# Kernel tuning notes

Measured on AMD Instinct MI355X. Metric: run time of the kernel, lower is better.

## Reference

```python
import jax, jax.numpy as jnp
import numpy as np

B, S, E, H = 1, 4096, 768, 12
D = E // H  # head_dim = 64


def setup_inputs() -> dict:
    key = jax.random.key(0)
    ks = jax.random.split(key, 9)
    s = 1.0 / np.sqrt(E)
    return {
        "x": jax.random.normal(ks[0], (B, S, E), dtype=jnp.float32),
        "Wq": jax.random.uniform(ks[1], (E, E), jnp.float32, -s, s),
        "bq": jax.random.uniform(ks[2], (E,), jnp.float32, -s, s),
        "Wk": jax.random.uniform(ks[3], (E, E), jnp.float32, -s, s),
        "bk": jax.random.uniform(ks[4], (E,), jnp.float32, -s, s),
        "Wv": jax.random.uniform(ks[5], (E, E), jnp.float32, -s, s),
        "bv": jax.random.uniform(ks[6], (E,), jnp.float32, -s, s),
        "Wo": jax.random.uniform(ks[7], (E, E), jnp.float32, -s, s),
        "bo": jax.random.uniform(ks[8], (E,), jnp.float32, -s, s),
    }


def reference(x, Wq, bq, Wk, bk, Wv, bv, Wo, bo):
    b, s, e = x.shape
    # QKV projections, split heads -> [b, h, s, d]
    def split(t):
        return t.reshape(b, s, H, D).transpose(0, 2, 1, 3)
    q = split(x @ Wq.T + bq)
    k = split(x @ Wk.T + bk)
    v = split(x @ Wv.T + bv)
    scores = jnp.einsum("bhqd,bhkd->bhqk", q, k) / jnp.sqrt(jnp.float32(D))
    attn = jax.nn.softmax(scores, axis=-1)  # dropout is identity in eval
    out = jnp.einsum("bhqk,bhkd->bhqd", attn, v)
    out = out.transpose(0, 2, 1, 3).reshape(b, s, e)
    return out @ Wo.T + bo
```

## Files before the change

kernel.cpp:

```cpp
#include <hip/hip_runtime.h>
#include <hip/hip_bf16.h>
#include <math.h>

#define SEQ 4096
#define EDIM 768
#define NHEAD 12
#define HDIM 64
#define SE (SEQ * EDIM)
#define WMAT (EDIM * EDIM)
#define QSCALE 0.180336880111f

typedef __attribute__((ext_vector_type(8))) __bf16 bf16x8;
typedef __attribute__((ext_vector_type(4))) float f32x4;
typedef __attribute__((ext_vector_type(8))) unsigned short u16x8;
typedef __attribute__((ext_vector_type(4))) unsigned short u16x4;
typedef unsigned short ushort_t;
typedef unsigned int uint_t;

#define MFMA16(a, b, c) __builtin_amdgcn_mfma_f32_16x16x32_bf16(a, b, c, 0, 0, 0)
#define GLOAD_LDS16(g, l)                                          \
  __builtin_amdgcn_global_load_lds(                                \
      (const __attribute__((address_space(1))) void*)(g),          \
      (__attribute__((address_space(3))) void*)(l), 16, 0, 0)

__device__ __forceinline__ unsigned short bfbits(float x) {
  return __builtin_bit_cast(unsigned short, (__bf16)x);
}
__device__ __forceinline__ void split1(float x, unsigned short* h,
                                       unsigned short* l) {
  __bf16 hb = (__bf16)x;
  *h = __builtin_bit_cast(unsigned short, hb);
  *l = __builtin_bit_cast(unsigned short, (__bf16)(x - (float)hb));
}
__device__ __forceinline__ bf16x8 ones8() {
  u16x8 u;
#pragma unroll
  for (int e = 0; e < 8; ++e) u[e] = 0x3F80;
  return __builtin_bit_cast(bf16x8, u);
}
__device__ __forceinline__ float exp2_hw(float x) {
  float r;
  asm("v_exp_f32 %0, %1" : "=v"(r) : "v"(x));
  return r;
}

__global__ __launch_bounds__(256) void wprep_kernel(
    const float* __restrict__ W0, const float* __restrict__ W1,
    const float* __restrict__ W2, const float* __restrict__ W3,
    ushort_t* __restrict__ WB, ushort_t* __restrict__ WOH,
    ushort_t* __restrict__ WOL) {
  const int m = blockIdx.y;
  const float* src = (m == 0) ? W0 : (m == 1) ? W1 : (m == 2) ? W2 : W3;
  const size_t i = ((size_t)blockIdx.x * 256 + threadIdx.x) * 8;
  float4 a = *(const float4*)(src + i);
  float4 b = *(const float4*)(src + i + 4);
  float fv[8] = {a.x, a.y, a.z, a.w, b.x, b.y, b.z, b.w};
  if (m < 3) {
    u16x8 hh;
#pragma unroll
    for (int e = 0; e < 8; ++e) hh[e] = bfbits(fv[e]);
    *(u16x8*)(WB + (size_t)m * WMAT + i) = hh;
  } else {
    u16x8 hh, ll;
#pragma unroll
    for (int e = 0; e < 8; ++e) {
      unsigned short x, y;
      split1(fv[e], &x, &y);
      hh[e] = x;
      ll[e] = y;
    }
    *(u16x8*)(WOH + i) = hh;
    *(u16x8*)(WOL + i) = ll;
  }
}

__global__ __launch_bounds__(256) void xprep_kernel(
    const float* __restrict__ x, ushort_t* __restrict__ xb) {
  const size_t i = ((size_t)blockIdx.x * 256 + threadIdx.x) * 8;
  float4 a = *(const float4*)(x + i);
  float4 b = *(const float4*)(x + i + 4);
  float fv[8] = {a.x, a.y, a.z, a.w, b.x, b.y, b.z, b.w};
  u16x8 hh;
#pragma unroll
  for (int e = 0; e < 8; ++e) hh[e] = bfbits(fv[e]);
  *(u16x8*)(xb + i) = hh;
}

__global__ __launch_bounds__(256) void qkv_kernel(
    const ushort_t* __restrict__ XB, const ushort_t* __restrict__ WB,
    const float* __restrict__ bq, const float* __restrict__ bk,
    const float* __restrict__ bv, ushort_t* __restrict__ QB,
    ushort_t* __restrict__ KB, ushort_t* __restrict__ VT) {
  __shared__ __align__(16) ushort_t AS[128][32];
  __shared__ __align__(16) ushort_t BS[128][32];

  const int z = blockIdx.z;
  const ushort_t* Bmat = WB + (size_t)z * WMAT;
  const float* bias = (z == 0) ? bq : (z == 1) ? bk : bv;
  ushort_t* outp = (z == 0) ? QB : (z == 1) ? KB : VT;
  const float scale = (z == 0) ? QSCALE : 1.0f;

  const int t = threadIdx.x;
  const int lane = t & 63;
  const int w = t >> 6;
  const int tn = t & 15;
  const int g = (t >> 4) & 3;
  const int wr = w >> 1, wc = w & 1;
  const int m0 = blockIdx.x * 128;
  const int n0 = blockIdx.y * 128;

  f32x4 acc[4][4];
#pragma unroll
  for (int mi = 0; mi < 4; ++mi)
#pragma unroll
    for (int nj = 0; nj < 4; ++nj) acc[mi][nj] = (f32x4){0.f, 0.f, 0.f, 0.f};

  const int crow = lane >> 2;
  const int ccol = (lane & 3) * 8;

  for (int k0 = 0; k0 < EDIM; k0 += 32) {
    __syncthreads();
#pragma unroll
    for (int i = 0; i < 2; ++i) {
      const int ch = w + 4 * i;
      const int row = ch * 16 + crow;
      GLOAD_LDS16(XB + (size_t)(m0 + row) * EDIM + k0 + ccol, &AS[ch * 16][0]);
      GLOAD_LDS16(Bmat + (size_t)(n0 + row) * EDIM + k0 + ccol, &BS[ch * 16][0]);
    }
    __syncthreads();

    bf16x8 ah[4], bh[4];
#pragma unroll
    for (int mi = 0; mi < 4; ++mi)
      ah[mi] = __builtin_bit_cast(
          bf16x8, *(const u16x8*)&AS[wr * 64 + mi * 16 + tn][8 * g]);
#pragma unroll
    for (int nj = 0; nj < 4; ++nj)
      bh[nj] = __builtin_bit_cast(
          bf16x8, *(const u16x8*)&BS[wc * 64 + nj * 16 + tn][8 * g]);
#pragma unroll
    for (int mi = 0; mi < 4; ++mi)
#pragma unroll
      for (int nj = 0; nj < 4; ++nj)
        acc[mi][nj] = MFMA16(ah[mi], bh[nj], acc[mi][nj]);
  }

#pragma unroll
  for (int mi = 0; mi < 4; ++mi) {
    const int rb = m0 + wr * 64 + mi * 16 + 4 * g;
#pragma unroll
    for (int nj = 0; nj < 4; ++nj) {
      const int col = n0 + wc * 64 + nj * 16 + tn;
      const float bb = bias[col];
      if (z == 2) {
        u16x4 pk;
#pragma unroll
        for (int r = 0; r < 4; ++r) pk[r] = bfbits(acc[mi][nj][r] + bb);
        *(u16x4*)(outp + (size_t)col * SEQ + rb) = pk;
      } else {
#pragma unroll
        for (int r = 0; r < 4; ++r)
          outp[(size_t)(rb + r) * EDIM + col] =
              bfbits((acc[mi][nj][r] + bb) * scale);
      }
    }
  }
}

__global__ __launch_bounds__(256) void proj_kernel(
    const ushort_t* __restrict__ Ah, const ushort_t* __restrict__ Al,
    const ushort_t* __restrict__ Bh, const ushort_t* __restrict__ Bl,
    const float* __restrict__ bias, float* __restrict__ outf) {
  __shared__ __align__(16) ushort_t AhS[128][32];
  __shared__ __align__(16) ushort_t AlS[128][32];
  __shared__ __align__(16) ushort_t BhS[128][32];
  __shared__ __align__(16) ushort_t BlS[128][32];

  const int t = threadIdx.x;
  const int lane = t & 63;
  const int w = t >> 6;
  const int tn = t & 15;
  const int g = (t >> 4) & 3;
  const int wr = w >> 1, wc = w & 1;
  const int m0 = blockIdx.x * 128;
  const int n0 = blockIdx.y * 128;

  f32x4 acc[4][4];
#pragma unroll
  for (int mi = 0; mi < 4; ++mi)
#pragma unroll
    for (int nj = 0; nj < 4; ++nj) acc[mi][nj] = (f32x4){0.f, 0.f, 0.f, 0.f};

  const int crow = lane >> 2;
  const int ccol = (lane & 3) * 8;

  for (int k0 = 0; k0 < EDIM; k0 += 32) {
    __syncthreads();
#pragma unroll
    for (int i = 0; i < 2; ++i) {
      const int ch = w + 4 * i;
      const int row = ch * 16 + crow;
      const size_t ga = (size_t)(m0 + row) * EDIM + k0 + ccol;
      const size_t gb = (size_t)(n0 + row) * EDIM + k0 + ccol;
      GLOAD_LDS16(Ah + ga, &AhS[ch * 16][0]);
      GLOAD_LDS16(Al + ga, &AlS[ch * 16][0]);
      GLOAD_LDS16(Bh + gb, &BhS[ch * 16][0]);
      GLOAD_LDS16(Bl + gb, &BlS[ch * 16][0]);
    }
    __syncthreads();

    bf16x8 ah[4], al[4], bh[4], bl[4];
#pragma unroll
    for (int mi = 0; mi < 4; ++mi) {
      ah[mi] = __builtin_bit_cast(
          bf16x8, *(const u16x8*)&AhS[wr * 64 + mi * 16 + tn][8 * g]);
      al[mi] = __builtin_bit_cast(
          bf16x8, *(const u16x8*)&AlS[wr * 64 + mi * 16 + tn][8 * g]);
    }
#pragma unroll
    for (int nj = 0; nj < 4; ++nj) {
      bh[nj] = __builtin_bit_cast(
          bf16x8, *(const u16x8*)&BhS[wc * 64 + nj * 16 + tn][8 * g]);
      bl[nj] = __builtin_bit_cast(
          bf16x8, *(const u16x8*)&BlS[wc * 64 + nj * 16 + tn][8 * g]);
    }
#pragma unroll
    for (int mi = 0; mi < 4; ++mi)
#pragma unroll
      for (int nj = 0; nj < 4; ++nj)
        acc[mi][nj] = MFMA16(ah[mi], bh[nj], acc[mi][nj]);
#pragma unroll
    for (int mi = 0; mi < 4; ++mi)
#pragma unroll
      for (int nj = 0; nj < 4; ++nj)
        acc[mi][nj] = MFMA16(al[mi], bh[nj], acc[mi][nj]);
#pragma unroll
    for (int mi = 0; mi < 4; ++mi)
#pragma unroll
      for (int nj = 0; nj < 4; ++nj)
        acc[mi][nj] = MFMA16(ah[mi], bl[nj], acc[mi][nj]);
  }

#pragma unroll
  for (int mi = 0; mi < 4; ++mi) {
    const int rb = m0 + wr * 64 + mi * 16 + 4 * g;
#pragma unroll
    for (int nj = 0; nj < 4; ++nj) {
      const int col = n0 + wc * 64 + nj * 16 + tn;
      const float bb = bias[col];
#pragma unroll
      for (int r = 0; r < 4; ++r)
        outf[(size_t)(rb + r) * EDIM + col] = acc[mi][nj][r] + bb;
    }
  }
}

__global__ __launch_bounds__(256) void attn_kernel(
    const ushort_t* __restrict__ QB, const ushort_t* __restrict__ KBg,
    const ushort_t* __restrict__ VTg, ushort_t* __restrict__ Ch_g,
    ushort_t* __restrict__ Cl_g) {
  __shared__ __align__(16) ushort_t KS[2][64][64];
  __shared__ __align__(16) ushort_t VS[2][64][64];
  __shared__ __align__(16) ushort_t Ps[4][16][72];

  const int t = threadIdx.x;
  const int lane = t & 63;
  const int tn = t & 15;
  const int g = (t >> 4) & 3;
  const int kg = g * 8;
  const int wid = t >> 6;
  const int h = blockIdx.y;
  const int q0 = blockIdx.x * 64;
  const int hoff = h * HDIM;

  bf16x8 qb[2];
  {
    const size_t qoff = (size_t)(q0 + 16 * wid + tn) * EDIM + hoff;
    qb[0] = __builtin_bit_cast(bf16x8, *(const u16x8*)(QB + qoff + kg));
    qb[1] = __builtin_bit_cast(bf16x8, *(const u16x8*)(QB + qoff + 32 + kg));
  }

  const int srow = lane >> 3;
  const int sxor = ((lane & 7) ^ srow) << 4;
  const int rswz = (tn & 7) << 4;
  const int off0 = (16 * g) ^ rswz;
  const int off1 = (64 + 16 * g) ^ rswz;

  const bf16x8 ones = ones8();
  f32x4 o[4], lsum;
#pragma unroll
  for (int j = 0; j < 4; ++j) o[j] = (f32x4){0.f, 0.f, 0.f, 0.f};
  lsum = (f32x4){0.f, 0.f, 0.f, 0.f};

#pragma unroll
  for (int c = 0; c < 2; ++c) {
    const int row = 16 * wid + 8 * c + srow;
    GLOAD_LDS16((const char*)(KBg + (size_t)row * EDIM + hoff) + sxor,
                &KS[0][16 * wid + 8 * c][0]);
    GLOAD_LDS16((const char*)(VTg + (size_t)(hoff + row) * SEQ) + sxor,
                &VS[0][16 * wid + 8 * c][0]);
  }

  for (int it = 0; it < SEQ / 64; ++it) {
    const int buf = it & 1;
    __syncthreads();

    if (it + 1 < SEQ / 64) {
      const int k0n = (it + 1) * 64;
#pragma unroll
      for (int c = 0; c < 2; ++c) {
        const int row = 16 * wid + 8 * c + srow;
        GLOAD_LDS16(
            (const char*)(KBg + (size_t)(k0n + row) * EDIM + hoff) + sxor,
            &KS[buf ^ 1][16 * wid + 8 * c][0]);
        GLOAD_LDS16(
            (const char*)(VTg + (size_t)(hoff + row) * SEQ + k0n) + sxor,
            &VS[buf ^ 1][16 * wid + 8 * c][0]);
      }
    }

    f32x4 s[4];
#pragma unroll
    for (int kb = 0; kb < 4; ++kb) {
      const char* krow = (const char*)&KS[buf][16 * kb + tn][0];
      const bf16x8 ka =
          __builtin_bit_cast(bf16x8, *(const u16x8*)(krow + off0));
      const bf16x8 kc =
          __builtin_bit_cast(bf16x8, *(const u16x8*)(krow + off1));
      s[kb] = (f32x4){0.f, 0.f, 0.f, 0.f};
      s[kb] = MFMA16(ka, qb[0], s[kb]);
      s[kb] = MFMA16(kc, qb[1], s[kb]);
    }

#pragma unroll
    for (int kb = 0; kb < 4; ++kb) {
      uint2 pk;
      pk.x = (uint_t)bfbits(exp2_hw(s[kb][0])) |
             ((uint_t)bfbits(exp2_hw(s[kb][1])) << 16);
      pk.y = (uint_t)bfbits(exp2_hw(s[kb][2])) |
             ((uint_t)bfbits(exp2_hw(s[kb][3])) << 16);
      *(uint2*)&Ps[wid][tn][16 * kb + 4 * g] = pk;
    }

    const bf16x8 pa0 =
        __builtin_bit_cast(bf16x8, *(const u16x8*)&Ps[wid][tn][kg]);
    const bf16x8 pa1 =
        __builtin_bit_cast(bf16x8, *(const u16x8*)&Ps[wid][tn][32 + kg]);

#pragma unroll
    for (int j = 0; j < 4; ++j) {
      const char* vrow = (const char*)&VS[buf][16 * j + tn][0];
      const bf16x8 v0 =
          __builtin_bit_cast(bf16x8, *(const u16x8*)(vrow + off0));
      const bf16x8 v1 =
          __builtin_bit_cast(bf16x8, *(const u16x8*)(vrow + off1));
      o[j] = MFMA16(pa0, v0, o[j]);
      o[j] = MFMA16(pa1, v1, o[j]);
    }
    lsum = MFMA16(pa0, ones, lsum);
    lsum = MFMA16(pa1, ones, lsum);
  }

#pragma unroll
  for (int r = 0; r < 4; ++r) {
    const float inv = 1.f / lsum[r];
#pragma unroll
    for (int j = 0; j < 4; ++j) {
      const float val = o[j][r] * inv;
      unsigned short hh, ll;
      split1(val, &hh, &ll);
      const size_t idx =
          (size_t)(q0 + 16 * wid + 4 * g + r) * EDIM + hoff + 16 * j + tn;
      Ch_g[idx] = hh;
      Cl_g[idx] = ll;
    }
  }
}

extern "C" void kernel_launch(void* const* d_in, const int* in_sizes, int n_in,
                              void* d_out, int out_size, void* d_ws,
                              size_t ws_size, hipStream_t stream) {
  const float* x  = (const float*)d_in[0];
  const float* Wq = (const float*)d_in[1];
  const float* bq = (const float*)d_in[2];
  const float* Wk = (const float*)d_in[3];
  const float* bk = (const float*)d_in[4];
  const float* Wv = (const float*)d_in[5];
  const float* bv = (const float*)d_in[6];
  const float* Wo = (const float*)d_in[7];
  const float* bo = (const float*)d_in[8];
  float* out = (float*)d_out;

  ushort_t* WB  = (ushort_t*)d_ws;
  ushort_t* WOH = WB + (size_t)3 * WMAT;
  ushort_t* WOL = WOH + (size_t)WMAT;
  ushort_t* XB  = WOL + (size_t)WMAT;
  ushort_t* QB  = XB + (size_t)SE;
  ushort_t* KB  = QB + (size_t)SE;
  ushort_t* VT  = KB + (size_t)SE;
  ushort_t* CH  = VT + (size_t)SE;
  ushort_t* CL  = CH + (size_t)SE;

  dim3 gw(WMAT / 2048, 4);
  wprep_kernel<<<gw, 256, 0, stream>>>(Wq, Wk, Wv, Wo, WB, WOH, WOL);
  xprep_kernel<<<SE / 2048, 256, 0, stream>>>(x, XB);

  dim3 gq(SEQ / 128, EDIM / 128, 3);
  qkv_kernel<<<gq, 256, 0, stream>>>(XB, WB, bq, bk, bv, QB, KB, VT);

  dim3 ga(SEQ / 64, NHEAD);
  attn_kernel<<<ga, 256, 0, stream>>>(QB, KB, VT, CH, CL);

  dim3 go(SEQ / 128, EDIM / 128);
  proj_kernel<<<go, 256, 0, stream>>>(CH, CL, WOH, WOL, bo, out);
}
```

Before: 164.4 us.

## Split attention key tile across wave pairs, 2x2 q/k warp layout with LDS reduction

Reorganizes the attention kernel so each wave handles 32 queries and half of each 64-key tile, instead of 16 queries over all keys. K and V fragments are reused across two query blocks, which halves LDS reads per MFMA. Partial outputs and row sums from the two key-halves are combined through shared memory at the end. This costs an extra reduction phase, two barriers, more accumulator registers and a larger LDS footprint that may reduce occupancy.

```diff
diff --git a/kernel.cpp b/kernel.cpp
--- a/kernel.cpp
+++ b/kernel.cpp
@@ -259,9 +259,10 @@
     const ushort_t* __restrict__ QB, const ushort_t* __restrict__ KBg,
     const ushort_t* __restrict__ VTg, ushort_t* __restrict__ Ch_g,
     ushort_t* __restrict__ Cl_g) {
-  __shared__ __align__(16) ushort_t KS[2][64][64];
-  __shared__ __align__(16) ushort_t VS[2][64][64];
-  __shared__ __align__(16) ushort_t Ps[4][16][72];
+  __shared__ __align__(16) char SMEM[43008];
+  ushort_t(*KS)[64][64] = (ushort_t(*)[64][64])SMEM;
+  ushort_t(*VS)[64][64] = (ushort_t(*)[64][64])(SMEM + 16384);
+  ushort_t(*Ps)[2][16][40] = (ushort_t(*)[2][16][40])(SMEM + 32768);
 
   const int t = threadIdx.x;
   const int lane = t & 63;
@@ -269,15 +270,19 @@
   const int g = (t >> 4) & 3;
   const int kg = g * 8;
   const int wid = t >> 6;
+  const int wq = wid & 1;
+  const int wk = wid >> 1;
   const int h = blockIdx.y;
   const int q0 = blockIdx.x * 64;
   const int hoff = h * HDIM;
 
-  bf16x8 qb[2];
-  {
-    const size_t qoff = (size_t)(q0 + 16 * wid + tn) * EDIM + hoff;
-    qb[0] = __builtin_bit_cast(bf16x8, *(const u16x8*)(QB + qoff + kg));
-    qb[1] = __builtin_bit_cast(bf16x8, *(const u16x8*)(QB + qoff + 32 + kg));
+  bf16x8 qbf[2][2];
+#pragma unroll
+  for (int qb = 0; qb < 2; ++qb) {
+    const ushort_t* qp =
+        QB + (size_t)(q0 + 32 * wq + 16 * qb + tn) * EDIM + hoff;
+    qbf[qb][0] = __builtin_bit_cast(bf16x8, *(const u16x8*)(qp + kg));
+    qbf[qb][1] = __builtin_bit_cast(bf16x8, *(const u16x8*)(qp + 32 + kg));
   }
 
   const int srow = lane >> 3;
@@ -285,12 +290,16 @@
   const int rswz = (tn & 7) << 4;
   const int off0 = (16 * g) ^ rswz;
   const int off1 = (64 + 16 * g) ^ rswz;
+  const int offv = (64 * wk + 16 * g) ^ rswz;
 
   const bf16x8 ones = ones8();
-  f32x4 o[4], lsum;
-#pragma unroll
-  for (int j = 0; j < 4; ++j) o[j] = (f32x4){0.f, 0.f, 0.f, 0.f};
-  lsum = (f32x4){0.f, 0.f, 0.f, 0.f};
+  f32x4 o[4][2], lsum[2];
+#pragma unroll
+  for (int qb = 0; qb < 2; ++qb) {
+    lsum[qb] = (f32x4){0.f, 0.f, 0.f, 0.f};
+#pragma unroll
+    for (int j = 0; j < 4; ++j) o[j][qb] = (f32x4){0.f, 0.f, 0.f, 0.f};
+  }
 
 #pragma unroll
   for (int c = 0; c < 2; ++c) {
@@ -319,60 +328,97 @@
       }
     }
 
-    f32x4 s[4];
-#pragma unroll
-    for (int kb = 0; kb < 4; ++kb) {
-      const char* krow = (const char*)&KS[buf][16 * kb + tn][0];
+    f32x4 s[2][2];
+#pragma unroll
+    for (int kb = 0; kb < 2; ++kb) {
+      const char* krow = (const char*)&KS[buf][32 * wk + 16 * kb + tn][0];
       const bf16x8 ka =
           __builtin_bit_cast(bf16x8, *(const u16x8*)(krow + off0));
       const bf16x8 kc =
           __builtin_bit_cast(bf16x8, *(const u16x8*)(krow + off1));
-      s[kb] = (f32x4){0.f, 0.f, 0.f, 0.f};
-      s[kb] = MFMA16(ka, qb[0], s[kb]);
-      s[kb] = MFMA16(kc, qb[1], s[kb]);
-    }
-
-#pragma unroll
-    for (int kb = 0; kb < 4; ++kb) {
-      uint2 pk;
-      pk.x = (uint_t)bfbits(exp2_hw(s[kb][0])) |
-             ((uint_t)bfbits(exp2_hw(s[kb][1])) << 16);
-      pk.y = (uint_t)bfbits(exp2_hw(s[kb][2])) |
-             ((uint_t)bfbits(exp2_hw(s[kb][3])) << 16);
-      *(uint2*)&Ps[wid][tn][16 * kb + 4 * g] = pk;
-    }
+#pragma unroll
+      for (int qb = 0; qb < 2; ++qb) {
+        s[kb][qb] = (f32x4){0.f, 0.f, 0.f, 0.f};
+        s[kb][qb] = MFMA16(ka, qbf[qb][0], s[kb][qb]);
+        s[kb][qb] = MFMA16(kc, qbf[qb][1], s[kb][qb]);
+      }
+    }
+
+#pragma unroll
+    for (int kb = 0; kb < 2; ++kb)
+#pragma unroll
+      for (int qb = 0; qb < 2; ++qb) {
+        uint2 pk;
+        pk.x = (uint_t)bfbits(exp2_hw(s[kb][qb][0])) |
+               ((uint_t)bfbits(exp2_hw(s[kb][qb][1])) << 16);
+        pk.y = (uint_t)bfbits(exp2_hw(s[kb][qb][2])) |
+               ((uint_t)bfbits(exp2_hw(s[kb][qb][3])) << 16);
+        *(uint2*)&Ps[wid][qb][tn][16 * kb + 4 * g] = pk;
+      }
 
     const bf16x8 pa0 =
-        __builtin_bit_cast(bf16x8, *(const u16x8*)&Ps[wid][tn][kg]);
+        __builtin_bit_cast(bf16x8, *(const u16x8*)&Ps[wid][0][tn][kg]);
     const bf16x8 pa1 =
-        __builtin_bit_cast(bf16x8, *(const u16x8*)&Ps[wid][tn][32 + kg]);
+        __builtin_bit_cast(bf16x8, *(const u16x8*)&Ps[wid][1][tn][kg]);
 
 #pragma unroll
     for (int j = 0; j < 4; ++j) {
       const char* vrow = (const char*)&VS[buf][16 * j + tn][0];
-      const bf16x8 v0 =
-          __builtin_bit_cast(bf16x8, *(const u16x8*)(vrow + off0));
-      const bf16x8 v1 =
-          __builtin_bit_cast(bf16x8, *(const u16x8*)(vrow + off1));
-      o[j] = MFMA16(pa0, v0, o[j]);
-      o[j] = MFMA16(pa1, v1, o[j]);
-    }
-    lsum = MFMA16(pa0, ones, lsum);
-    lsum = MFMA16(pa1, ones, lsum);
-  }
-
-#pragma unroll
-  for (int r = 0; r < 4; ++r) {
-    const float inv = 1.f / lsum[r];
-#pragma unroll
-    for (int j = 0; j < 4; ++j) {
-      const float val = o[j][r] * inv;
-      unsigned short hh, ll;
-      split1(val, &hh, &ll);
-      const size_t idx =
-          (size_t)(q0 + 16 * wid + 4 * g + r) * EDIM + hoff + 16 * j + tn;
-      Ch_g[idx] = hh;
-      Cl_g[idx] = ll;
+      const bf16x8 vf =
+          __builtin_bit_cast(bf16x8, *(const u16x8*)(vrow + offv));
+      o[j][0] = MFMA16(pa0, vf, o[j][0]);
+      o[j][1] = MFMA16(pa1, vf, o[j][1]);
+    }
+    lsum[0] = MFMA16(pa0, ones, lsum[0]);
+    lsum[1] = MFMA16(pa1, ones, lsum[1]);
+  }
+
+  float(*Of)[68] = (float(*)[68])SMEM;
+  float* Lf = (float*)(SMEM + 17408);
+
+  __syncthreads();
+  if (wk == 1) {
+#pragma unroll
+    for (int qb = 0; qb < 2; ++qb) {
+#pragma unroll
+      for (int j = 0; j < 4; ++j)
+        *(float4*)&Of[16 * j + tn][32 * wq + 16 * qb + 4 * g] =
+            make_float4(o[j][qb][0], o[j][qb][1], o[j][qb][2], o[j][qb][3]);
+      if (tn == 0) {
+#pragma unroll
+        for (int r = 0; r < 4; ++r)
+          Lf[32 * wq + 16 * qb + 4 * g + r] = lsum[qb][r];
+      }
+    }
+  }
+  __syncthreads();
+  if (wk == 0) {
+#pragma unroll
+    for (int qb = 0; qb < 2; ++qb) {
+      float linv[4];
+#pragma unroll
+      for (int r = 0; r < 4; ++r)
+        linv[r] =
+            1.f / (lsum[qb][r] + Lf[32 * wq + 16 * qb + 4 * g + r]);
+#pragma unroll
+      for (int j = 0; j < 4; ++j) {
+        const float4 ov =
+            *(const float4*)&Of[16 * j + tn][32 * wq + 16 * qb + 4 * g];
+        const float vals[4] = {(o[j][qb][0] + ov.x) * linv[0],
+                               (o[j][qb][1] + ov.y) * linv[1],
+                               (o[j][qb][2] + ov.z) * linv[2],
+                               (o[j][qb][3] + ov.w) * linv[3]};
+#pragma unroll
+        for (int r = 0; r < 4; ++r) {
+          unsigned short hh, ll;
+          split1(vals[r], &hh, &ll);
+          const size_t idx =
+              (size_t)(q0 + 32 * wq + 16 * qb + 4 * g + r) * EDIM + hoff +
+              16 * j + tn;
+          Ch_g[idx] = hh;
+          Cl_g[idx] = ll;
+        }
+      }
     }
   }
 }
```

After: 158.6 us. 3.5% less time.
